# Optimization experiments

Measured on AMD Instinct MI355X. Metric: run time of the kernel, lower is better.

## Reference

```python
import jax, jax.numpy as jnp
import numpy as np

B, D_IN, D_H, H = 8192, 1024, 1024, 4
HD = D_H // H          # 256 head dim
D_P = int(D_H * 4 / 3) # 1365 projection dim


def setup_inputs() -> dict:
    key = jax.random.key(0)
    ks = jax.random.split(key, 16)
    s = 0.02
    inp = {
        'x': jax.random.normal(ks[0], (B, D_IN), jnp.float32),
        'h_prev': jnp.zeros((B, D_H), jnp.float32),
        'c_prev': jnp.zeros((B, D_H), jnp.float32),
        'n_prev': jnp.zeros((B, D_H), jnp.float32),
        'm_prev': jnp.zeros((B, D_H), jnp.float32),
        'ln_w': jnp.ones((D_IN,), jnp.float32),
        'ln_b': jnp.zeros((D_IN,), jnp.float32),
        'Wz': jax.random.normal(ks[1], (D_IN, D_H)) * s,
        'bz': jnp.zeros((D_H,)),
        'Wi': jax.random.normal(ks[2], (D_IN, D_H)) * s,
        'bi': jnp.zeros((D_H,)),
        'Wf': jax.random.normal(ks[3], (D_IN, D_H)) * s,
        'bf': jnp.zeros((D_H,)),
        'Wo': jax.random.normal(ks[4], (D_IN, D_H)) * s,
        'bo': jnp.zeros((D_H,)),
        'Rz': jax.random.normal(ks[5], (H, HD, HD)) * s,
        'rbz': jnp.zeros((D_H,)),
        'Ri': jax.random.normal(ks[6], (H, HD, HD)) * s,
        'rbi': jnp.zeros((D_H,)),
        'Rf': jax.random.normal(ks[7], (H, HD, HD)) * s,
        'rbf': jnp.zeros((D_H,)),
        'Ro': jax.random.normal(ks[8], (H, HD, HD)) * s,
        'rbo': jnp.zeros((D_H,)),
        'gn_w': jnp.ones((D_H,)),
        'gn_b': jnp.zeros((D_H,)),
        'Wup': jax.random.normal(ks[9], (D_H, 2 * D_P)) * s,
        'bup': jnp.zeros((2 * D_P,)),
        'Wdown': jax.random.normal(ks[10], (D_P, D_IN)) * s,
        'bdown': jnp.zeros((D_IN,)),
    }
    return inp


def reference(x, h_prev, c_prev, n_prev, m_prev,
              ln_w, ln_b,
              Wz, bz, Wi, bi, Wf, bf, Wo, bo,
              Rz, rbz, Ri, rbi, Rf, rbf, Ro, rbo,
              gn_w, gn_b, Wup, bup, Wdown, bdown):
    EPS = 1e-5
    # LayerNorm over input_dim
    mu = x.mean(-1, keepdims=True)
    var = x.var(-1, keepdims=True)
    x_oz = (x - mu) / jnp.sqrt(var + EPS) * ln_w + ln_b
    x_fi = x_oz  # use_conv=False

    # block-diagonal recurrence: per-head (HD x HD) matmul
    hr = h_prev.reshape(B, H, HD)
    def blk(R, rb):
        return jnp.einsum('bhd,hde->bhe', hr, R).reshape(B, D_H) + rb

    z_t = x_oz @ Wz + bz + blk(Rz, rbz)
    i_t = x_fi @ Wi + bi + blk(Ri, rbi)
    f_t = x_fi @ Wf + bf + blk(Rf, rbf)
    o_t = x_fi @ Wo + bo + blk(Ro, rbo)

    zt = jnp.tanh(z_t)
    ot = jax.nn.sigmoid(o_t)
    mt = jnp.maximum(f_t + m_prev, i_t)          # stabilizer
    it = jnp.exp(i_t - mt)
    ft = jnp.exp(f_t + m_prev - mt)
    ct = ft * c_prev + it * zt
    nt = ft * n_prev + it
    ht = ot * (ct / (nt + 1e-13))

    # GroupNorm(num_heads, hidden_dim) on (B, D_H)
    g = ht.reshape(B, H, HD)
    gm = g.mean(-1, keepdims=True)
    gv = g.var(-1, keepdims=True)
    ht_norm = ((g - gm) / jnp.sqrt(gv + EPS)).reshape(B, D_H) * gn_w + gn_b

    # GeGLU feedforward + residual
    up = ht_norm @ Wup + bup
    s_, g_ = up[:, :D_P], up[:, D_P:]
    y = (s_ * jax.nn.gelu(g_, approximate=False)) @ Wdown + bdown + x
    return (y, ht, ct, nt, mt)
```

## Files before the change

### kernel.cpp

```cpp
#include <hip/hip_runtime.h>
#include <hip/hip_bf16.h>
#include <math.h>

#define B_ROWS 8192
#define DIN    1024
#define DH     1024
#define HD     256
#define DP     1365
#define DP2    2730
#define NUP    2816
#define KDN    1408

typedef __bf16 bf16x8 __attribute__((ext_vector_type(8)));
typedef float  f32x4  __attribute__((ext_vector_type(4)));
typedef unsigned short ushort_t;

__device__ __forceinline__ unsigned short f2bf(float f) {
    union { __hip_bfloat16 b; unsigned short u; } v; v.b = __float2bfloat16(f); return v.u;
}
__device__ __forceinline__ float bf2f(unsigned short u) {
    union { __hip_bfloat16 b; unsigned short u; } v; v.u = u; return __bfloat162float(v.b);
}

__global__ __launch_bounds__(256) void prep_hprev(const float* __restrict__ hp,
                                                  ushort_t* __restrict__ out) {
    size_t i = ((size_t)blockIdx.x * 256 + threadIdx.x) * 8;
    float4 a = *(const float4*)(hp + i);
    float4 b = *(const float4*)(hp + i + 4);
    union { unsigned short s[8]; uint4 v; } o;
    o.s[0] = f2bf(a.x); o.s[1] = f2bf(a.y); o.s[2] = f2bf(a.z); o.s[3] = f2bf(a.w);
    o.s[4] = f2bf(b.x); o.s[5] = f2bf(b.y); o.s[6] = f2bf(b.z); o.s[7] = f2bf(b.w);
    *(uint4*)(out + i) = o.v;
}

__global__ __launch_bounds__(256) void prep_wgates(
    const float* __restrict__ Wz, const float* __restrict__ Wi,
    const float* __restrict__ Wf, const float* __restrict__ Wo,
    const float* __restrict__ Rz, const float* __restrict__ Ri,
    const float* __restrict__ Rf, const float* __restrict__ Ro,
    ushort_t* __restrict__ WT) {
    int g = blockIdx.z;
    const float* W = (g == 0) ? Wz : (g == 1) ? Wi : (g == 2) ? Wf : Wo;
    const float* R = (g == 0) ? Rz : (g == 1) ? Ri : (g == 2) ? Rf : Ro;
    int n  = blockIdx.x * 256 + threadIdx.x;
    int k0 = blockIdx.y * 8;
    union { unsigned short s[8]; uint4 v; } o;
    if (k0 < 1024) {
        #pragma unroll
        for (int j = 0; j < 8; ++j) o.s[j] = f2bf(W[(size_t)(k0 + j) * DH + n]);
    } else {
        int h = n >> 8, e = n & 255, d0 = k0 - 1024;
        #pragma unroll
        for (int j = 0; j < 8; ++j) o.s[j] = f2bf(R[h * 65536 + (d0 + j) * 256 + e]);
    }
    *(uint4*)(WT + (size_t)g * 1024 * 1280 + (size_t)n * 1280 + k0) = o.v;
}

__global__ __launch_bounds__(256) void prep_wup(const float* __restrict__ Wup,
                                                ushort_t* __restrict__ WupT) {
    int n  = blockIdx.x * 256 + threadIdx.x;
    int k0 = blockIdx.y * 8;
    union { unsigned short s[8]; uint4 v; } o;
    #pragma unroll
    for (int j = 0; j < 8; ++j)
        o.s[j] = (n < DP2) ? f2bf(Wup[(size_t)(k0 + j) * DP2 + n]) : (unsigned short)0;
    *(uint4*)(WupT + (size_t)n * 1024 + k0) = o.v;
}

__global__ __launch_bounds__(256) void prep_wdown(const float* __restrict__ Wdown,
                                                  ushort_t* __restrict__ WdnT) {
    int n  = blockIdx.x * 256 + threadIdx.x;
    int k0 = blockIdx.y * 8;
    union { unsigned short s[8]; uint4 v; } o;
    #pragma unroll
    for (int j = 0; j < 8; ++j) {
        int k = k0 + j;
        o.s[j] = (k < DP) ? f2bf(Wdown[(size_t)k * DIN + n]) : (unsigned short)0;
    }
    *(uint4*)(WdnT + (size_t)n * KDN + k0) = o.v;
}

__global__ __launch_bounds__(256) void ln_kernel(const float* __restrict__ x,
                                                 const float* __restrict__ w,
                                                 const float* __restrict__ b,
                                                 ushort_t* __restrict__ xn) {
    int row = blockIdx.x;
    int tid = threadIdx.x;
    const float4 v = *(const float4*)(x + (size_t)row * DIN + tid * 4);
    float s  = v.x + v.y + v.z + v.w;
    float sq = v.x*v.x + v.y*v.y + v.z*v.z + v.w*v.w;
    #pragma unroll
    for (int off = 32; off; off >>= 1) {
        s  += __shfl_xor(s, off);
        sq += __shfl_xor(sq, off);
    }
    __shared__ float ss[8];
    int wid = tid >> 6, lane = tid & 63;
    if (lane == 0) { ss[wid] = s; ss[4 + wid] = sq; }
    __syncthreads();
    s  = ss[0] + ss[1] + ss[2] + ss[3];
    sq = ss[4] + ss[5] + ss[6] + ss[7];
    float mu  = s * (1.0f / DIN);
    float var = sq * (1.0f / DIN) - mu * mu;
    float inv = rsqrtf(var + 1e-5f);
    int c = tid * 4;
    float4 wv = *(const float4*)(w + c);
    float4 bv = *(const float4*)(b + c);
    union { unsigned short s4[4]; uint2 v2; } o;
    o.s4[0] = f2bf((v.x - mu) * inv * wv.x + bv.x);
    o.s4[1] = f2bf((v.y - mu) * inv * wv.y + bv.y);
    o.s4[2] = f2bf((v.z - mu) * inv * wv.z + bv.z);
    o.s4[3] = f2bf((v.w - mu) * inv * wv.w + bv.w);
    *(uint2*)(xn + (size_t)row * DIN + c) = o.v2;
}

__global__ __launch_bounds__(256) void gemm_gates_bf(
    const ushort_t* __restrict__ xn, const ushort_t* __restrict__ hp,
    const ushort_t* __restrict__ WT,
    const float* __restrict__ bz, const float* __restrict__ bi,
    const float* __restrict__ bf_, const float* __restrict__ bo,
    const float* __restrict__ rbz, const float* __restrict__ rbi,
    const float* __restrict__ rbf, const float* __restrict__ rbo,
    ushort_t* __restrict__ gates) {
    int g = blockIdx.z;
    const float* bias = (g == 0) ? bz  : (g == 1) ? bi  : (g == 2) ? bf_ : bo;
    const float* rb   = (g == 0) ? rbz : (g == 1) ? rbi : (g == 2) ? rbf : rbo;
    const ushort_t* Wg = WT + (size_t)g * 1024 * 1280;

    __shared__ __align__(16) ushort_t As[128 * 32];
    __shared__ __align__(16) ushort_t Bs[128 * 32];
    int tid = threadIdx.x, lane = tid & 63, wave = tid >> 6;
    int wm = wave >> 1, wn = wave & 1;
    int m0 = blockIdx.y * 128, n0 = blockIdx.x * 128;
    int head = n0 >> 8;
    int trow = tid >> 2;
    int tk   = (tid & 3) * 8;
    int l15 = lane & 15, l4 = lane >> 4;

    f32x4 acc[4][4];
    #pragma unroll
    for (int i = 0; i < 4; ++i)
        #pragma unroll
        for (int j = 0; j < 4; ++j) acc[i][j] = (f32x4){0.f, 0.f, 0.f, 0.f};

    for (int kt = 0; kt < 40; ++kt) {
        int k0 = kt * 32;
        const ushort_t* ap = (k0 < 1024) ? xn + k0
                                         : hp + head * 256 + (k0 - 1024);
        bf16x8 a0 = *(const bf16x8*)(ap + (size_t)(m0 + trow) * 1024 + tk);
        bf16x8 a1 = *(const bf16x8*)(ap + (size_t)(m0 + trow + 64) * 1024 + tk);
        bf16x8 b0 = *(const bf16x8*)(Wg + (size_t)(n0 + trow) * 1280 + k0 + tk);
        bf16x8 b1 = *(const bf16x8*)(Wg + (size_t)(n0 + trow + 64) * 1280 + k0 + tk);
        __syncthreads();
        *(bf16x8*)(As + trow * 32 + tk)        = a0;
        *(bf16x8*)(As + (trow + 64) * 32 + tk) = a1;
        *(bf16x8*)(Bs + trow * 32 + tk)        = b0;
        *(bf16x8*)(Bs + (trow + 64) * 32 + tk) = b1;
        __syncthreads();
        bf16x8 af[4], bv[4];
        #pragma unroll
        for (int i = 0; i < 4; ++i) {
            af[i] = *(const bf16x8*)(As + (wm * 64 + i * 16 + l15) * 32 + l4 * 8);
            bv[i] = *(const bf16x8*)(Bs + (wn * 64 + i * 16 + l15) * 32 + l4 * 8);
        }
        #pragma unroll
        for (int mi = 0; mi < 4; ++mi)
            #pragma unroll
            for (int ni = 0; ni < 4; ++ni)
                acc[mi][ni] = __builtin_amdgcn_mfma_f32_16x16x32_bf16(af[mi], bv[ni], acc[mi][ni], 0, 0, 0);
    }

    ushort_t* og = gates + (size_t)g * B_ROWS * DH;
    #pragma unroll
    for (int ni = 0; ni < 4; ++ni) {
        int col = n0 + wn * 64 + ni * 16 + l15;
        float badd = bias[col] + rb[col];
        #pragma unroll
        for (int mi = 0; mi < 4; ++mi) {
            int rbase = m0 + wm * 64 + mi * 16 + l4 * 4;
            #pragma unroll
            for (int j = 0; j < 4; ++j)
                og[(size_t)(rbase + j) * DH + col] = f2bf(acc[mi][ni][j] + badd);
        }
    }
}

__global__ __launch_bounds__(256) void pointwise_gn(
    const ushort_t* __restrict__ gbf,
    const float* __restrict__ c_prev, const float* __restrict__ n_prev,
    const float* __restrict__ m_prev, const float* __restrict__ gn_w,
    const float* __restrict__ gn_b, float* __restrict__ out,
    ushort_t* __restrict__ htn) {
    int row = blockIdx.x;
    int tid = threadIdx.x;
    int head = tid >> 6, lane = tid & 63;
    int col = head * HD + lane * 4;
    size_t idx = (size_t)row * DH + col;
    const size_t N = (size_t)B_ROWS * DH;

    float zv[4], ivv[4], fv[4], ov[4];
    {
        union { uint2 v; unsigned short s[4]; } t;
        t.v = *(const uint2*)(gbf + idx);
        for (int j = 0; j < 4; ++j) zv[j] = bf2f(t.s[j]);
        t.v = *(const uint2*)(gbf + N + idx);
        for (int j = 0; j < 4; ++j) ivv[j] = bf2f(t.s[j]);
        t.v = *(const uint2*)(gbf + 2 * N + idx);
        for (int j = 0; j < 4; ++j) fv[j] = bf2f(t.s[j]);
        t.v = *(const uint2*)(gbf + 3 * N + idx);
        for (int j = 0; j < 4; ++j) ov[j] = bf2f(t.s[j]);
    }
    float4 cp = *(const float4*)(c_prev + idx);
    float4 np = *(const float4*)(n_prev + idx);
    float4 mp = *(const float4*)(m_prev + idx);
    float cpv[4] = {cp.x, cp.y, cp.z, cp.w};
    float npv[4] = {np.x, np.y, np.z, np.w};
    float mpv[4] = {mp.x, mp.y, mp.z, mp.w};

    float htv[4], ctv[4], ntv[4], mtv[4];
    float s = 0.f, sq = 0.f;
    #pragma unroll
    for (int j = 0; j < 4; ++j) {
        float zt = tanhf(zv[j]);
        float ot = 1.0f / (1.0f + expf(-ov[j]));
        float mt = fmaxf(fv[j] + mpv[j], ivv[j]);
        float it = expf(ivv[j] - mt);
        float ft = expf(fv[j] + mpv[j] - mt);
        float ct = ft * cpv[j] + it * zt;
        float nt = ft * npv[j] + it;
        float h  = ot * (ct / (nt + 1e-13f));
        htv[j] = h; ctv[j] = ct; ntv[j] = nt; mtv[j] = mt;
        s += h; sq += h * h;
    }
    *(float4*)(out + N     + idx) = make_float4(htv[0], htv[1], htv[2], htv[3]);
    *(float4*)(out + 2 * N + idx) = make_float4(ctv[0], ctv[1], ctv[2], ctv[3]);
    *(float4*)(out + 3 * N + idx) = make_float4(ntv[0], ntv[1], ntv[2], ntv[3]);
    *(float4*)(out + 4 * N + idx) = make_float4(mtv[0], mtv[1], mtv[2], mtv[3]);

    #pragma unroll
    for (int off = 1; off < 64; off <<= 1) {
        s  += __shfl_xor(s, off);
        sq += __shfl_xor(sq, off);
    }
    float mean = s * (1.0f / HD);
    float var  = fmaxf(sq * (1.0f / HD) - mean * mean, 0.0f);
    float inv  = rsqrtf(var + 1e-5f);
    float4 gw = *(const float4*)(gn_w + col);
    float4 gb = *(const float4*)(gn_b + col);
    float gwv[4] = {gw.x, gw.y, gw.z, gw.w};
    float gbv[4] = {gb.x, gb.y, gb.z, gb.w};
    union { unsigned short s4[4]; uint2 v2; } o;
    #pragma unroll
    for (int j = 0; j < 4; ++j)
        o.s4[j] = f2bf((htv[j] - mean) * inv * gwv[j] + gbv[j]);
    *(uint2*)(htn + idx) = o.v2;
}

__global__ __launch_bounds__(256) void gemm_up_bf(const ushort_t* __restrict__ htn,
                                                  const ushort_t* __restrict__ WupT,
                                                  const float* __restrict__ bup,
                                                  ushort_t* __restrict__ up) {
    __shared__ __align__(16) ushort_t As[128 * 32];
    __shared__ __align__(16) ushort_t Bs[128 * 32];
    int tid = threadIdx.x, lane = tid & 63, wave = tid >> 6;
    int wm = wave >> 1, wn = wave & 1;
    int m0 = blockIdx.y * 128, n0 = blockIdx.x * 128;
    int trow = tid >> 2;
    int tk   = (tid & 3) * 8;
    int l15 = lane & 15, l4 = lane >> 4;

    f32x4 acc[4][4];
    #pragma unroll
    for (int i = 0; i < 4; ++i)
        #pragma unroll
        for (int j = 0; j < 4; ++j) acc[i][j] = (f32x4){0.f, 0.f, 0.f, 0.f};

    for (int kt = 0; kt < 32; ++kt) {
        int k0 = kt * 32;
        bf16x8 a0 = *(const bf16x8*)(htn  + (size_t)(m0 + trow) * 1024 + k0 + tk);
        bf16x8 a1 = *(const bf16x8*)(htn  + (size_t)(m0 + trow + 64) * 1024 + k0 + tk);
        bf16x8 b0 = *(const bf16x8*)(WupT + (size_t)(n0 + trow) * 1024 + k0 + tk);
        bf16x8 b1 = *(const bf16x8*)(WupT + (size_t)(n0 + trow + 64) * 1024 + k0 + tk);
        __syncthreads();
        *(bf16x8*)(As + trow * 32 + tk)        = a0;
        *(bf16x8*)(As + (trow + 64) * 32 + tk) = a1;
        *(bf16x8*)(Bs + trow * 32 + tk)        = b0;
        *(bf16x8*)(Bs + (trow + 64) * 32 + tk) = b1;
        __syncthreads();
        bf16x8 af[4], bv[4];
        #pragma unroll
        for (int i = 0; i < 4; ++i) {
            af[i] = *(const bf16x8*)(As + (wm * 64 + i * 16 + l15) * 32 + l4 * 8);
            bv[i] = *(const bf16x8*)(Bs + (wn * 64 + i * 16 + l15) * 32 + l4 * 8);
        }
        #pragma unroll
        for (int mi = 0; mi < 4; ++mi)
            #pragma unroll
            for (int ni = 0; ni < 4; ++ni)
                acc[mi][ni] = __builtin_amdgcn_mfma_f32_16x16x32_bf16(af[mi], bv[ni], acc[mi][ni], 0, 0, 0);
    }

    #pragma unroll
    for (int ni = 0; ni < 4; ++ni) {
        int col = n0 + wn * 64 + ni * 16 + l15;
        float badd = (col < DP2) ? bup[col] : 0.f;
        #pragma unroll
        for (int mi = 0; mi < 4; ++mi) {
            int rbase = m0 + wm * 64 + mi * 16 + l4 * 4;
            #pragma unroll
            for (int j = 0; j < 4; ++j)
                up[(size_t)(rbase + j) * NUP + col] = f2bf(acc[mi][ni][j] + badd);
        }
    }
}

__global__ __launch_bounds__(256) void gelu_kernel(const ushort_t* __restrict__ up,
                                                   ushort_t* __restrict__ act) {
    int row = blockIdx.y;
    int c = blockIdx.x * 256 + threadIdx.x;
    if (c >= KDN) return;
    float v = 0.f;
    if (c < DP) {
        float s = bf2f(up[(size_t)row * NUP + c]);
        float g = bf2f(up[(size_t)row * NUP + DP + c]);
        v = s * 0.5f * g * (1.0f + erff(g * 0.70710678118654752f));
    }
    act[(size_t)row * KDN + c] = f2bf(v);
}

__global__ __launch_bounds__(256) void gemm_down_bf(const ushort_t* __restrict__ act,
                                                    const ushort_t* __restrict__ WdnT,
                                                    const float* __restrict__ bdown,
                                                    const float* __restrict__ x,
                                                    float* __restrict__ y) {
    __shared__ __align__(16) ushort_t As[128 * 32];
    __shared__ __align__(16) ushort_t Bs[128 * 32];
    int tid = threadIdx.x, lane = tid & 63, wave = tid >> 6;
    int wm = wave >> 1, wn = wave & 1;
    int m0 = blockIdx.y * 128, n0 = blockIdx.x * 128;
    int trow = tid >> 2;
    int tk   = (tid & 3) * 8;
    int l15 = lane & 15, l4 = lane >> 4;

    f32x4 acc[4][4];
    #pragma unroll
    for (int i = 0; i < 4; ++i)
        #pragma unroll
        for (int j = 0; j < 4; ++j) acc[i][j] = (f32x4){0.f, 0.f, 0.f, 0.f};

    for (int kt = 0; kt < 44; ++kt) {
        int k0 = kt * 32;
        bf16x8 a0 = *(const bf16x8*)(act  + (size_t)(m0 + trow) * KDN + k0 + tk);
        bf16x8 a1 = *(const bf16x8*)(act  + (size_t)(m0 + trow + 64) * KDN + k0 + tk);
        bf16x8 b0 = *(const bf16x8*)(WdnT + (size_t)(n0 + trow) * KDN + k0 + tk);
        bf16x8 b1 = *(const bf16x8*)(WdnT + (size_t)(n0 + trow + 64) * KDN + k0 + tk);
        __syncthreads();
        *(bf16x8*)(As + trow * 32 + tk)        = a0;
        *(bf16x8*)(As + (trow + 64) * 32 + tk) = a1;
        *(bf16x8*)(Bs + trow * 32 + tk)        = b0;
        *(bf16x8*)(Bs + (trow + 64) * 32 + tk) = b1;
        __syncthreads();
        bf16x8 af[4], bv[4];
        #pragma unroll
        for (int i = 0; i < 4; ++i) {
            af[i] = *(const bf16x8*)(As + (wm * 64 + i * 16 + l15) * 32 + l4 * 8);
            bv[i] = *(const bf16x8*)(Bs + (wn * 64 + i * 16 + l15) * 32 + l4 * 8);
        }
        #pragma unroll
        for (int mi = 0; mi < 4; ++mi)
            #pragma unroll
            for (int ni = 0; ni < 4; ++ni)
                acc[mi][ni] = __builtin_amdgcn_mfma_f32_16x16x32_bf16(af[mi], bv[ni], acc[mi][ni], 0, 0, 0);
    }

    #pragma unroll
    for (int ni = 0; ni < 4; ++ni) {
        int col = n0 + wn * 64 + ni * 16 + l15;
        float bd = bdown[col];
        #pragma unroll
        for (int mi = 0; mi < 4; ++mi) {
            int rbase = m0 + wm * 64 + mi * 16 + l4 * 4;
            #pragma unroll
            for (int j = 0; j < 4; ++j) {
                int r = rbase + j;
                y[(size_t)r * DIN + col] = acc[mi][ni][j] + bd + x[(size_t)r * DIN + col];
            }
        }
    }
}

extern "C" void kernel_launch(void* const* d_in, const int* in_sizes, int n_in,
                              void* d_out, int out_size, void* d_ws, size_t ws_size,
                              hipStream_t stream) {
    (void)in_sizes; (void)n_in; (void)out_size; (void)ws_size;
    const float* x      = (const float*)d_in[0];
    const float* h_prev = (const float*)d_in[1];
    const float* c_prev = (const float*)d_in[2];
    const float* n_prev = (const float*)d_in[3];
    const float* m_prev = (const float*)d_in[4];
    const float* ln_w   = (const float*)d_in[5];
    const float* ln_b   = (const float*)d_in[6];
    const float* Wz = (const float*)d_in[7];  const float* bz = (const float*)d_in[8];
    const float* Wi = (const float*)d_in[9];  const float* bi = (const float*)d_in[10];
    const float* Wf = (const float*)d_in[11]; const float* bf_ = (const float*)d_in[12];
    const float* Wo = (const float*)d_in[13]; const float* bo = (const float*)d_in[14];
    const float* Rz = (const float*)d_in[15]; const float* rbz = (const float*)d_in[16];
    const float* Ri = (const float*)d_in[17]; const float* rbi = (const float*)d_in[18];
    const float* Rf = (const float*)d_in[19]; const float* rbf = (const float*)d_in[20];
    const float* Ro = (const float*)d_in[21]; const float* rbo = (const float*)d_in[22];
    const float* gn_w = (const float*)d_in[23]; const float* gn_b = (const float*)d_in[24];
    const float* Wup  = (const float*)d_in[25]; const float* bup  = (const float*)d_in[26];
    const float* Wdown = (const float*)d_in[27]; const float* bdown = (const float*)d_in[28];

    char* w = (char*)d_ws;
    ushort_t* hp_bf  = (ushort_t*)(w);
    ushort_t* WTg    = (ushort_t*)(w + 16777216);
    ushort_t* WupT   = (ushort_t*)(w + 27262976);
    ushort_t* WdnT   = (ushort_t*)(w + 33030144);
    ushort_t* xn_bf  = (ushort_t*)(w + 35913728);
    ushort_t* htn_bf = xn_bf;
    char*     big    = w + 52690944;
    ushort_t* gates_bf = (ushort_t*)big;
    ushort_t* up_bf    = (ushort_t*)big;
    ushort_t* act_bf   = (ushort_t*)(big + 46137344);
    float* out = (float*)d_out;

    prep_hprev <<<4096, 256, 0, stream>>>(h_prev, hp_bf);
    prep_wgates<<<dim3(4, 160, 4), 256, 0, stream>>>(Wz, Wi, Wf, Wo, Rz, Ri, Rf, Ro, WTg);
    prep_wup   <<<dim3(11, 128), 256, 0, stream>>>(Wup, WupT);
    prep_wdown <<<dim3(4, 176), 256, 0, stream>>>(Wdown, WdnT);
    ln_kernel  <<<B_ROWS, 256, 0, stream>>>(x, ln_w, ln_b, xn_bf);

    gemm_gates_bf<<<dim3(8, 64, 4), 256, 0, stream>>>(
        xn_bf, hp_bf, WTg, bz, bi, bf_, bo, rbz, rbi, rbf, rbo, gates_bf);

    pointwise_gn<<<B_ROWS, 256, 0, stream>>>(
        gates_bf, c_prev, n_prev, m_prev, gn_w, gn_b, out, htn_bf);

    gemm_up_bf<<<dim3(22, 64), 256, 0, stream>>>(htn_bf, WupT, bup, up_bf);

    gelu_kernel<<<dim3(6, B_ROWS), 256, 0, stream>>>(up_bf, act_bf);

    gemm_down_bf<<<dim3(8, 64), 256, 0, stream>>>(act_bf, WdnT, bdown, x, out);
}
```

Measured before the change: 673.8 us.

## Double-buffer LDS in GEMM kernels, swizzle LDS layout, remap workgroups for L2 locality

All three bf16 MFMA GEMMs now use two LDS buffers, so the global loads for the next k-tile are issued before the MFMAs on the current tile, and there is one barrier per tile instead of two. The LDS layout is changed to a k-group-major arrangement so that fragment reads and writes are contiguous 16-byte chunks, which is meant to cut bank conflicts. Block indices are remapped to interleave workgroups across what appear to be XCDs (stride 8), so that neighbouring tiles share L2. The cost is double the LDS footprint and more live registers, which may reduce occupancy.

```diff
diff --git a/kernel.cpp b/kernel.cpp
--- a/kernel.cpp
+++ b/kernel.cpp
@@ -114,6 +114,7 @@
     *(uint2*)(xn + (size_t)row * DIN + c) = o.v2;
 }
 
+
 __global__ __launch_bounds__(256) void gemm_gates_bf(
     const ushort_t* __restrict__ xn, const ushort_t* __restrict__ hp,
     const ushort_t* __restrict__ WT,
@@ -122,20 +123,25 @@
     const float* __restrict__ rbz, const float* __restrict__ rbi,
     const float* __restrict__ rbf, const float* __restrict__ rbo,
     ushort_t* __restrict__ gates) {
-    int g = blockIdx.z;
+    int bid = blockIdx.x + (blockIdx.y << 3) + (blockIdx.z << 9);
+    int wgs = (bid & 7) * 256 + (bid >> 3);
+    int bxi = wgs & 7, rest = wgs >> 3, byi = rest & 63;
+    int g   = rest >> 6;
     const float* bias = (g == 0) ? bz  : (g == 1) ? bi  : (g == 2) ? bf_ : bo;
     const float* rb   = (g == 0) ? rbz : (g == 1) ? rbi : (g == 2) ? rbf : rbo;
     const ushort_t* Wg = WT + (size_t)g * 1024 * 1280;
 
-    __shared__ __align__(16) ushort_t As[128 * 32];
-    __shared__ __align__(16) ushort_t Bs[128 * 32];
+    __shared__ __align__(16) char Ash[2][8192];
+    __shared__ __align__(16) char Bsh[2][8192];
     int tid = threadIdx.x, lane = tid & 63, wave = tid >> 6;
     int wm = wave >> 1, wn = wave & 1;
-    int m0 = blockIdx.y * 128, n0 = blockIdx.x * 128;
+    int m0 = byi * 128, n0 = bxi * 128;
     int head = n0 >> 8;
-    int trow = tid >> 2;
-    int tk   = (tid & 3) * 8;
+    int trow = tid >> 2, kg = tid & 3, tk = kg * 8;
     int l15 = lane & 15, l4 = lane >> 4;
+    int wa  = ((trow >> 4) << 10) + (kg << 8) + ((trow & 15) << 4);
+    int raA = (wm << 12) + (l4 << 8) + (l15 << 4);
+    int raB = (wn << 12) + (l4 << 8) + (l15 << 4);
 
     f32x4 acc[4][4];
     #pragma unroll
@@ -143,31 +149,56 @@
         #pragma unroll
         for (int j = 0; j < 4; ++j) acc[i][j] = (f32x4){0.f, 0.f, 0.f, 0.f};
 
-    for (int kt = 0; kt < 40; ++kt) {
-        int k0 = kt * 32;
-        const ushort_t* ap = (k0 < 1024) ? xn + k0
-                                         : hp + head * 256 + (k0 - 1024);
-        bf16x8 a0 = *(const bf16x8*)(ap + (size_t)(m0 + trow) * 1024 + tk);
-        bf16x8 a1 = *(const bf16x8*)(ap + (size_t)(m0 + trow + 64) * 1024 + tk);
-        bf16x8 b0 = *(const bf16x8*)(Wg + (size_t)(n0 + trow) * 1280 + k0 + tk);
-        bf16x8 b1 = *(const bf16x8*)(Wg + (size_t)(n0 + trow + 64) * 1280 + k0 + tk);
-        __syncthreads();
-        *(bf16x8*)(As + trow * 32 + tk)        = a0;
-        *(bf16x8*)(As + (trow + 64) * 32 + tk) = a1;
-        *(bf16x8*)(Bs + trow * 32 + tk)        = b0;
-        *(bf16x8*)(Bs + (trow + 64) * 32 + tk) = b1;
-        __syncthreads();
+    const ushort_t* aX = xn + (size_t)(m0 + trow) * 1024 + tk;
+    const ushort_t* aH = hp + (size_t)(m0 + trow) * 1024 + head * 256 + tk;
+    const ushort_t* bW = Wg + (size_t)(n0 + trow) * 1280 + tk;
+
+    auto loadAB = [&](int kt, bf16x8& a0, bf16x8& a1, bf16x8& b0, bf16x8& b1) {
+        const ushort_t* p = (kt < 32) ? aX + kt * 32 : aH + (kt - 32) * 32;
+        a0 = *(const bf16x8*)p;
+        a1 = *(const bf16x8*)(p + 64 * 1024);
+        const ushort_t* q = bW + kt * 32;
+        b0 = *(const bf16x8*)q;
+        b1 = *(const bf16x8*)(q + 64 * 1280);
+    };
+    auto stage = [&](char* A, char* Bb, bf16x8 a0, bf16x8 a1, bf16x8 b0, bf16x8 b1) {
+        *(bf16x8*)(A + wa)         = a0;
+        *(bf16x8*)(A + wa + 4096)  = a1;
+        *(bf16x8*)(Bb + wa)        = b0;
+        *(bf16x8*)(Bb + wa + 4096) = b1;
+    };
+    auto compute = [&](const char* A, const char* Bb) {
         bf16x8 af[4], bv[4];
         #pragma unroll
         for (int i = 0; i < 4; ++i) {
-            af[i] = *(const bf16x8*)(As + (wm * 64 + i * 16 + l15) * 32 + l4 * 8);
-            bv[i] = *(const bf16x8*)(Bs + (wn * 64 + i * 16 + l15) * 32 + l4 * 8);
+            af[i] = *(const bf16x8*)(A  + raA + i * 1024);
+            bv[i] = *(const bf16x8*)(Bb + raB + i * 1024);
         }
         #pragma unroll
         for (int mi = 0; mi < 4; ++mi)
             #pragma unroll
             for (int ni = 0; ni < 4; ++ni)
                 acc[mi][ni] = __builtin_amdgcn_mfma_f32_16x16x32_bf16(af[mi], bv[ni], acc[mi][ni], 0, 0, 0);
+    };
+
+    {
+        bf16x8 a0, a1, b0, b1;
+        loadAB(0, a0, a1, b0, b1);
+        stage(Ash[0], Bsh[0], a0, a1, b0, b1);
+    }
+    __syncthreads();
+    for (int kt = 0; kt < 40; kt += 2) {
+        bf16x8 a0, a1, b0, b1;
+        loadAB(kt + 1, a0, a1, b0, b1);
+        compute(Ash[0], Bsh[0]);
+        stage(Ash[1], Bsh[1], a0, a1, b0, b1);
+        __syncthreads();
+        if (kt + 2 < 40) loadAB(kt + 2, a0, a1, b0, b1);
+        compute(Ash[1], Bsh[1]);
+        if (kt + 2 < 40) {
+            stage(Ash[0], Bsh[0], a0, a1, b0, b1);
+            __syncthreads();
+        }
     }
 
     ushort_t* og = gates + (size_t)g * B_ROWS * DH;
@@ -260,14 +291,20 @@
                                                   const ushort_t* __restrict__ WupT,
                                                   const float* __restrict__ bup,
                                                   ushort_t* __restrict__ up) {
-    __shared__ __align__(16) ushort_t As[128 * 32];
-    __shared__ __align__(16) ushort_t Bs[128 * 32];
+    int bid = blockIdx.x + blockIdx.y * 22;
+    int wgs = (bid & 7) * 176 + (bid >> 3);
+    int bxi = wgs % 22, byi = wgs / 22;
+
+    __shared__ __align__(16) char Ash[2][8192];
+    __shared__ __align__(16) char Bsh[2][8192];
     int tid = threadIdx.x, lane = tid & 63, wave = tid >> 6;
     int wm = wave >> 1, wn = wave & 1;
-    int m0 = blockIdx.y * 128, n0 = blockIdx.x * 128;
-    int trow = tid >> 2;
-    int tk   = (tid & 3) * 8;
+    int m0 = byi * 128, n0 = bxi * 128;
+    int trow = tid >> 2, kg = tid & 3, tk = kg * 8;
     int l15 = lane & 15, l4 = lane >> 4;
+    int wa  = ((trow >> 4) << 10) + (kg << 8) + ((trow & 15) << 4);
+    int raA = (wm << 12) + (l4 << 8) + (l15 << 4);
+    int raB = (wn << 12) + (l4 << 8) + (l15 << 4);
 
     f32x4 acc[4][4];
     #pragma unroll
@@ -275,29 +312,55 @@
         #pragma unroll
         for (int j = 0; j < 4; ++j) acc[i][j] = (f32x4){0.f, 0.f, 0.f, 0.f};
 
-    for (int kt = 0; kt < 32; ++kt) {
-        int k0 = kt * 32;
-        bf16x8 a0 = *(const bf16x8*)(htn  + (size_t)(m0 + trow) * 1024 + k0 + tk);
-        bf16x8 a1 = *(const bf16x8*)(htn  + (size_t)(m0 + trow + 64) * 1024 + k0 + tk);
-        bf16x8 b0 = *(const bf16x8*)(WupT + (size_t)(n0 + trow) * 1024 + k0 + tk);
-        bf16x8 b1 = *(const bf16x8*)(WupT + (size_t)(n0 + trow + 64) * 1024 + k0 + tk);
-        __syncthreads();
-        *(bf16x8*)(As + trow * 32 + tk)        = a0;
-        *(bf16x8*)(As + (trow + 64) * 32 + tk) = a1;
-        *(bf16x8*)(Bs + trow * 32 + tk)        = b0;
-        *(bf16x8*)(Bs + (trow + 64) * 32 + tk) = b1;
-        __syncthreads();
+    const ushort_t* aP = htn  + (size_t)(m0 + trow) * 1024 + tk;
+    const ushort_t* bP = WupT + (size_t)(n0 + trow) * 1024 + tk;
+
+    auto loadAB = [&](int kt, bf16x8& a0, bf16x8& a1, bf16x8& b0, bf16x8& b1) {
+        const ushort_t* p = aP + kt * 32;
+        a0 = *(const bf16x8*)p;
+        a1 = *(const bf16x8*)(p + 64 * 1024);
+        const ushort_t* q = bP + kt * 32;
+        b0 = *(const bf16x8*)q;
+        b1 = *(const bf16x8*)(q + 64 * 1024);
+    };
+    auto stage = [&](char* A, char* Bb, bf16x8 a0, bf16x8 a1, bf16x8 b0, bf16x8 b1) {
+        *(bf16x8*)(A + wa)         = a0;
+        *(bf16x8*)(A + wa + 4096)  = a1;
+        *(bf16x8*)(Bb + wa)        = b0;
+        *(bf16x8*)(Bb + wa + 4096) = b1;
+    };
+    auto compute = [&](const char* A, const char* Bb) {
         bf16x8 af[4], bv[4];
         #pragma unroll
         for (int i = 0; i < 4; ++i) {
-            af[i] = *(const bf16x8*)(As + (wm * 64 + i * 16 + l15) * 32 + l4 * 8);
-            bv[i] = *(const bf16x8*)(Bs + (wn * 64 + i * 16 + l15) * 32 + l4 * 8);
+            af[i] = *(const bf16x8*)(A  + raA + i * 1024);
+            bv[i] = *(const bf16x8*)(Bb + raB + i * 1024);
         }
         #pragma unroll
         for (int mi = 0; mi < 4; ++mi)
             #pragma unroll
             for (int ni = 0; ni < 4; ++ni)
                 acc[mi][ni] = __builtin_amdgcn_mfma_f32_16x16x32_bf16(af[mi], bv[ni], acc[mi][ni], 0, 0, 0);
+    };
+
+    {
+        bf16x8 a0, a1, b0, b1;
+        loadAB(0, a0, a1, b0, b1);
+        stage(Ash[0], Bsh[0], a0, a1, b0, b1);
+    }
+    __syncthreads();
+    for (int kt = 0; kt < 32; kt += 2) {
+        bf16x8 a0, a1, b0, b1;
+        loadAB(kt + 1, a0, a1, b0, b1);
+        compute(Ash[0], Bsh[0]);
+        stage(Ash[1], Bsh[1], a0, a1, b0, b1);
+        __syncthreads();
+        if (kt + 2 < 32) loadAB(kt + 2, a0, a1, b0, b1);
+        compute(Ash[1], Bsh[1]);
+        if (kt + 2 < 32) {
+            stage(Ash[0], Bsh[0], a0, a1, b0, b1);
+            __syncthreads();
+        }
     }
 
     #pragma unroll
@@ -333,14 +396,20 @@
                                                     const float* __restrict__ bdown,
                                                     const float* __restrict__ x,
                                                     float* __restrict__ y) {
-    __shared__ __align__(16) ushort_t As[128 * 32];
-    __shared__ __align__(16) ushort_t Bs[128 * 32];
+    int bid = blockIdx.x + (blockIdx.y << 3);
+    int wgs = (bid & 7) * 64 + (bid >> 3);
+    int bxi = wgs & 7, byi = wgs >> 3;
+
+    __shared__ __align__(16) char Ash[2][8192];
+    __shared__ __align__(16) char Bsh[2][8192];
     int tid = threadIdx.x, lane = tid & 63, wave = tid >> 6;
     int wm = wave >> 1, wn = wave & 1;
-    int m0 = blockIdx.y * 128, n0 = blockIdx.x * 128;
-    int trow = tid >> 2;
-    int tk   = (tid & 3) * 8;
+    int m0 = byi * 128, n0 = bxi * 128;
+    int trow = tid >> 2, kg = tid & 3, tk = kg * 8;
     int l15 = lane & 15, l4 = lane >> 4;
+    int wa  = ((trow >> 4) << 10) + (kg << 8) + ((trow & 15) << 4);
+    int raA = (wm << 12) + (l4 << 8) + (l15 << 4);
+    int raB = (wn << 12) + (l4 << 8) + (l15 << 4);
 
     f32x4 acc[4][4];
     #pragma unroll
@@ -348,29 +417,55 @@
         #pragma unroll
         for (int j = 0; j < 4; ++j) acc[i][j] = (f32x4){0.f, 0.f, 0.f, 0.f};
 
-    for (int kt = 0; kt < 44; ++kt) {
-        int k0 = kt * 32;
-        bf16x8 a0 = *(const bf16x8*)(act  + (size_t)(m0 + trow) * KDN + k0 + tk);
-        bf16x8 a1 = *(const bf16x8*)(act  + (size_t)(m0 + trow + 64) * KDN + k0 + tk);
-        bf16x8 b0 = *(const bf16x8*)(WdnT + (size_t)(n0 + trow) * KDN + k0 + tk);
-        bf16x8 b1 = *(const bf16x8*)(WdnT + (size_t)(n0 + trow + 64) * KDN + k0 + tk);
-        __syncthreads();
-        *(bf16x8*)(As + trow * 32 + tk)        = a0;
-        *(bf16x8*)(As + (trow + 64) * 32 + tk) = a1;
-        *(bf16x8*)(Bs + trow * 32 + tk)        = b0;
-        *(bf16x8*)(Bs + (trow + 64) * 32 + tk) = b1;
-        __syncthreads();
+    const ushort_t* aP = act  + (size_t)(m0 + trow) * KDN + tk;
+    const ushort_t* bP = WdnT + (size_t)(n0 + trow) * KDN + tk;
+
+    auto loadAB = [&](int kt, bf16x8& a0, bf16x8& a1, bf16x8& b0, bf16x8& b1) {
+        const ushort_t* p = aP + kt * 32;
+        a0 = *(const bf16x8*)p;
+        a1 = *(const bf16x8*)(p + 64 * KDN);
+        const ushort_t* q = bP + kt * 32;
+        b0 = *(const bf16x8*)q;
+        b1 = *(const bf16x8*)(q + 64 * KDN);
+    };
+    auto stage = [&](char* A, char* Bb, bf16x8 a0, bf16x8 a1, bf16x8 b0, bf16x8 b1) {
+        *(bf16x8*)(A + wa)         = a0;
+        *(bf16x8*)(A + wa + 4096)  = a1;
+        *(bf16x8*)(Bb + wa)        = b0;
+        *(bf16x8*)(Bb + wa + 4096) = b1;
+    };
+    auto compute = [&](const char* A, const char* Bb) {
         bf16x8 af[4], bv[4];
         #pragma unroll
         for (int i = 0; i < 4; ++i) {
-            af[i] = *(const bf16x8*)(As + (wm * 64 + i * 16 + l15) * 32 + l4 * 8);
-            bv[i] = *(const bf16x8*)(Bs + (wn * 64 + i * 16 + l15) * 32 + l4 * 8);
+            af[i] = *(const bf16x8*)(A  + raA + i * 1024);
+            bv[i] = *(const bf16x8*)(Bb + raB + i * 1024);
         }
         #pragma unroll
         for (int mi = 0; mi < 4; ++mi)
             #pragma unroll
             for (int ni = 0; ni < 4; ++ni)
                 acc[mi][ni] = __builtin_amdgcn_mfma_f32_16x16x32_bf16(af[mi], bv[ni], acc[mi][ni], 0, 0, 0);
+    };
+
+    {
+        bf16x8 a0, a1, b0, b1;
+        loadAB(0, a0, a1, b0, b1);
+        stage(Ash[0], Bsh[0], a0, a1, b0, b1);
+    }
+    __syncthreads();
+    for (int kt = 0; kt < 44; kt += 2) {
+        bf16x8 a0, a1, b0, b1;
+        loadAB(kt + 1, a0, a1, b0, b1);
+        compute(Ash[0], Bsh[0]);
+        stage(Ash[1], Bsh[1], a0, a1, b0, b1);
+        __syncthreads();
+        if (kt + 2 < 44) loadAB(kt + 2, a0, a1, b0, b1);
+        compute(Ash[1], Bsh[1]);
+        if (kt + 2 < 44) {
+            stage(Ash[0], Bsh[0], a0, a1, b0, b1);
+            __syncthreads();
+        }
     }
 
     #pragma unroll
```

New measurement: 645.3 us. 4.2% less time.

## Use shared 256x256 double-buffered MFMA GEMM core with XCD-aware block remap

Applied to the files above, without the earlier changes.

Replaces the three 128x128 single-buffered GEMM kernels with a shared templated 256x256 tile core using 512 threads, 8 waves each computing 128x64. Shared memory is double-buffered so the next K-slice's global loads overlap the current MFMA compute, which drops one barrier per iteration. The LDS layout is swizzled into 16-row chunks, and a block-index remap groups neighbouring tiles onto the same XCD for L2 reuse. The larger tiles raise register pressure and cut grid size (e.g. 512 blocks for gates, 128 for down), which risks lower occupancy and tail effects.

```diff
diff --git a/kernel.cpp b/kernel.cpp
--- a/kernel.cpp
+++ b/kernel.cpp
@@ -114,7 +114,73 @@
     *(uint2*)(xn + (size_t)row * DIN + c) = o.v2;
 }
 
-__global__ __launch_bounds__(256) void gemm_gates_bf(
+template<int NK, int SW>
+__device__ __forceinline__ void gemm_core256(
+    const ushort_t* __restrict__ aP0, const ushort_t* __restrict__ aP1, int lda,
+    const ushort_t* __restrict__ bP, int ldb,
+    char* AshB, char* BshB, f32x4 (&acc)[8][4])
+{
+    int tid = threadIdx.x, lane = tid & 63, wave = tid >> 6;
+    int wm = wave >> 2, wn = wave & 3;
+    int trow = tid >> 1, koff = (tid & 1) * 16;
+    int l15 = lane & 15, l4 = lane >> 4;
+    int wA  = ((trow >> 4) << 10) + ((tid & 1) << 9) + ((trow & 15) << 4);
+    int raA = (wm << 13) + (l4 << 8) + (l15 << 4);
+    int raB = (wn << 12) + (l4 << 8) + (l15 << 4);
+    const ushort_t* aRow0 = aP0 + (size_t)trow * lda + koff;
+    const ushort_t* aRow1 = aP1 + (size_t)trow * lda + koff;
+    const ushort_t* bRow  = bP  + (size_t)trow * ldb + koff;
+
+    auto loadAB = [&](int kt, bf16x8& a0, bf16x8& a1, bf16x8& b0, bf16x8& b1) {
+        const ushort_t* p = (SW >= NK || kt < SW) ? aRow0 + kt * 32
+                                                  : aRow1 + (kt - SW) * 32;
+        a0 = *(const bf16x8*)p;
+        a1 = *(const bf16x8*)(p + 8);
+        const ushort_t* q = bRow + kt * 32;
+        b0 = *(const bf16x8*)q;
+        b1 = *(const bf16x8*)(q + 8);
+    };
+    auto stage = [&](char* A, char* B_, bf16x8 a0, bf16x8 a1, bf16x8 b0, bf16x8 b1) {
+        *(bf16x8*)(A + wA)        = a0;
+        *(bf16x8*)(A + wA + 256)  = a1;
+        *(bf16x8*)(B_ + wA)       = b0;
+        *(bf16x8*)(B_ + wA + 256) = b1;
+    };
+    auto compute = [&](const char* A, const char* B_) {
+        bf16x8 af[8], bv[4];
+        #pragma unroll
+        for (int i = 0; i < 8; ++i) af[i] = *(const bf16x8*)(A + raA + i * 1024);
+        #pragma unroll
+        for (int i = 0; i < 4; ++i) bv[i] = *(const bf16x8*)(B_ + raB + i * 1024);
+        #pragma unroll
+        for (int mi = 0; mi < 8; ++mi)
+            #pragma unroll
+            for (int ni = 0; ni < 4; ++ni)
+                acc[mi][ni] = __builtin_amdgcn_mfma_f32_16x16x32_bf16(af[mi], bv[ni], acc[mi][ni], 0, 0, 0);
+    };
+
+    {
+        bf16x8 a0, a1, b0, b1;
+        loadAB(0, a0, a1, b0, b1);
+        stage(AshB, BshB, a0, a1, b0, b1);
+    }
+    __syncthreads();
+    for (int kt = 0; kt < NK; kt += 2) {
+        bf16x8 a0, a1, b0, b1;
+        loadAB(kt + 1, a0, a1, b0, b1);
+        compute(AshB, BshB);
+        stage(AshB + 16384, BshB + 16384, a0, a1, b0, b1);
+        __syncthreads();
+        if (kt + 2 < NK) loadAB(kt + 2, a0, a1, b0, b1);
+        compute(AshB + 16384, BshB + 16384);
+        if (kt + 2 < NK) {
+            stage(AshB, BshB, a0, a1, b0, b1);
+            __syncthreads();
+        }
+    }
+}
+
+__global__ __launch_bounds__(512, 2) void gemm_gates_bf(
     const ushort_t* __restrict__ xn, const ushort_t* __restrict__ hp,
     const ushort_t* __restrict__ WT,
     const float* __restrict__ bz, const float* __restrict__ bi,
@@ -122,62 +188,38 @@
     const float* __restrict__ rbz, const float* __restrict__ rbi,
     const float* __restrict__ rbf, const float* __restrict__ rbo,
     ushort_t* __restrict__ gates) {
-    int g = blockIdx.z;
+    int bid = blockIdx.x + (blockIdx.y << 2) + (blockIdx.z << 7);
+    int wgs = (bid & 7) * 64 + (bid >> 3);
+    int bxi = wgs & 3, rest = wgs >> 2, byi = rest & 31, g = rest >> 5;
     const float* bias = (g == 0) ? bz  : (g == 1) ? bi  : (g == 2) ? bf_ : bo;
     const float* rb   = (g == 0) ? rbz : (g == 1) ? rbi : (g == 2) ? rbf : rbo;
     const ushort_t* Wg = WT + (size_t)g * 1024 * 1280;
-
-    __shared__ __align__(16) ushort_t As[128 * 32];
-    __shared__ __align__(16) ushort_t Bs[128 * 32];
-    int tid = threadIdx.x, lane = tid & 63, wave = tid >> 6;
-    int wm = wave >> 1, wn = wave & 1;
-    int m0 = blockIdx.y * 128, n0 = blockIdx.x * 128;
-    int head = n0 >> 8;
-    int trow = tid >> 2;
-    int tk   = (tid & 3) * 8;
+    int m0 = byi * 256, n0 = bxi * 256, head = bxi;
+
+    __shared__ __align__(16) char Ash[2][16384];
+    __shared__ __align__(16) char Bsh[2][16384];
+    f32x4 acc[8][4];
+    #pragma unroll
+    for (int i = 0; i < 8; ++i)
+        #pragma unroll
+        for (int j = 0; j < 4; ++j) acc[i][j] = (f32x4){0.f, 0.f, 0.f, 0.f};
+
+    gemm_core256<40, 32>(xn + (size_t)m0 * 1024,
+                         hp + (size_t)m0 * 1024 + head * 256, 1024,
+                         Wg + (size_t)n0 * 1280, 1280,
+                         &Ash[0][0], &Bsh[0][0], acc);
+
+    int lane = threadIdx.x & 63, wave = threadIdx.x >> 6;
+    int wm = wave >> 2, wn = wave & 3;
     int l15 = lane & 15, l4 = lane >> 4;
-
-    f32x4 acc[4][4];
-    #pragma unroll
-    for (int i = 0; i < 4; ++i)
-        #pragma unroll
-        for (int j = 0; j < 4; ++j) acc[i][j] = (f32x4){0.f, 0.f, 0.f, 0.f};
-
-    for (int kt = 0; kt < 40; ++kt) {
-        int k0 = kt * 32;
-        const ushort_t* ap = (k0 < 1024) ? xn + k0
-                                         : hp + head * 256 + (k0 - 1024);
-        bf16x8 a0 = *(const bf16x8*)(ap + (size_t)(m0 + trow) * 1024 + tk);
-        bf16x8 a1 = *(const bf16x8*)(ap + (size_t)(m0 + trow + 64) * 1024 + tk);
-        bf16x8 b0 = *(const bf16x8*)(Wg + (size_t)(n0 + trow) * 1280 + k0 + tk);
-        bf16x8 b1 = *(const bf16x8*)(Wg + (size_t)(n0 + trow + 64) * 1280 + k0 + tk);
-        __syncthreads();
-        *(bf16x8*)(As + trow * 32 + tk)        = a0;
-        *(bf16x8*)(As + (trow + 64) * 32 + tk) = a1;
-        *(bf16x8*)(Bs + trow * 32 + tk)        = b0;
-        *(bf16x8*)(Bs + (trow + 64) * 32 + tk) = b1;
-        __syncthreads();
-        bf16x8 af[4], bv[4];
-        #pragma unroll
-        for (int i = 0; i < 4; ++i) {
-            af[i] = *(const bf16x8*)(As + (wm * 64 + i * 16 + l15) * 32 + l4 * 8);
-            bv[i] = *(const bf16x8*)(Bs + (wn * 64 + i * 16 + l15) * 32 + l4 * 8);
-        }
-        #pragma unroll
-        for (int mi = 0; mi < 4; ++mi)
-            #pragma unroll
-            for (int ni = 0; ni < 4; ++ni)
-                acc[mi][ni] = __builtin_amdgcn_mfma_f32_16x16x32_bf16(af[mi], bv[ni], acc[mi][ni], 0, 0, 0);
-    }
-
     ushort_t* og = gates + (size_t)g * B_ROWS * DH;
     #pragma unroll
     for (int ni = 0; ni < 4; ++ni) {
         int col = n0 + wn * 64 + ni * 16 + l15;
         float badd = bias[col] + rb[col];
         #pragma unroll
-        for (int mi = 0; mi < 4; ++mi) {
-            int rbase = m0 + wm * 64 + mi * 16 + l4 * 4;
+        for (int mi = 0; mi < 8; ++mi) {
+            int rbase = m0 + wm * 128 + mi * 16 + l4 * 4;
             #pragma unroll
             for (int j = 0; j < 4; ++j)
                 og[(size_t)(rbase + j) * DH + col] = f2bf(acc[mi][ni][j] + badd);
@@ -256,57 +298,37 @@
     *(uint2*)(htn + idx) = o.v2;
 }
 
-__global__ __launch_bounds__(256) void gemm_up_bf(const ushort_t* __restrict__ htn,
-                                                  const ushort_t* __restrict__ WupT,
-                                                  const float* __restrict__ bup,
-                                                  ushort_t* __restrict__ up) {
-    __shared__ __align__(16) ushort_t As[128 * 32];
-    __shared__ __align__(16) ushort_t Bs[128 * 32];
-    int tid = threadIdx.x, lane = tid & 63, wave = tid >> 6;
-    int wm = wave >> 1, wn = wave & 1;
-    int m0 = blockIdx.y * 128, n0 = blockIdx.x * 128;
-    int trow = tid >> 2;
-    int tk   = (tid & 3) * 8;
+__global__ __launch_bounds__(512, 2) void gemm_up_bf(const ushort_t* __restrict__ htn,
+                                                     const ushort_t* __restrict__ WupT,
+                                                     const float* __restrict__ bup,
+                                                     ushort_t* __restrict__ up) {
+    int bid = blockIdx.x + blockIdx.y * 11;
+    int wgs = (bid & 7) * 44 + (bid >> 3);
+    int bxi = wgs % 11, byi = wgs / 11;
+    int m0 = byi * 256, n0 = bxi * 256;
+
+    __shared__ __align__(16) char Ash[2][16384];
+    __shared__ __align__(16) char Bsh[2][16384];
+    f32x4 acc[8][4];
+    #pragma unroll
+    for (int i = 0; i < 8; ++i)
+        #pragma unroll
+        for (int j = 0; j < 4; ++j) acc[i][j] = (f32x4){0.f, 0.f, 0.f, 0.f};
+
+    const ushort_t* aP = htn + (size_t)m0 * 1024;
+    gemm_core256<32, 32>(aP, aP, 1024, WupT + (size_t)n0 * 1024, 1024,
+                         &Ash[0][0], &Bsh[0][0], acc);
+
+    int lane = threadIdx.x & 63, wave = threadIdx.x >> 6;
+    int wm = wave >> 2, wn = wave & 3;
     int l15 = lane & 15, l4 = lane >> 4;
-
-    f32x4 acc[4][4];
-    #pragma unroll
-    for (int i = 0; i < 4; ++i)
-        #pragma unroll
-        for (int j = 0; j < 4; ++j) acc[i][j] = (f32x4){0.f, 0.f, 0.f, 0.f};
-
-    for (int kt = 0; kt < 32; ++kt) {
-        int k0 = kt * 32;
-        bf16x8 a0 = *(const bf16x8*)(htn  + (size_t)(m0 + trow) * 1024 + k0 + tk);
-        bf16x8 a1 = *(const bf16x8*)(htn  + (size_t)(m0 + trow + 64) * 1024 + k0 + tk);
-        bf16x8 b0 = *(const bf16x8*)(WupT + (size_t)(n0 + trow) * 1024 + k0 + tk);
-        bf16x8 b1 = *(const bf16x8*)(WupT + (size_t)(n0 + trow + 64) * 1024 + k0 + tk);
-        __syncthreads();
-        *(bf16x8*)(As + trow * 32 + tk)        = a0;
-        *(bf16x8*)(As + (trow + 64) * 32 + tk) = a1;
-        *(bf16x8*)(Bs + trow * 32 + tk)        = b0;
-        *(bf16x8*)(Bs + (trow + 64) * 32 + tk) = b1;
-        __syncthreads();
-        bf16x8 af[4], bv[4];
-        #pragma unroll
-        for (int i = 0; i < 4; ++i) {
-            af[i] = *(const bf16x8*)(As + (wm * 64 + i * 16 + l15) * 32 + l4 * 8);
-            bv[i] = *(const bf16x8*)(Bs + (wn * 64 + i * 16 + l15) * 32 + l4 * 8);
-        }
-        #pragma unroll
-        for (int mi = 0; mi < 4; ++mi)
-            #pragma unroll
-            for (int ni = 0; ni < 4; ++ni)
-                acc[mi][ni] = __builtin_amdgcn_mfma_f32_16x16x32_bf16(af[mi], bv[ni], acc[mi][ni], 0, 0, 0);
-    }
-
     #pragma unroll
     for (int ni = 0; ni < 4; ++ni) {
         int col = n0 + wn * 64 + ni * 16 + l15;
         float badd = (col < DP2) ? bup[col] : 0.f;
         #pragma unroll
-        for (int mi = 0; mi < 4; ++mi) {
-            int rbase = m0 + wm * 64 + mi * 16 + l4 * 4;
+        for (int mi = 0; mi < 8; ++mi) {
+            int rbase = m0 + wm * 128 + mi * 16 + l4 * 4;
             #pragma unroll
             for (int j = 0; j < 4; ++j)
                 up[(size_t)(rbase + j) * NUP + col] = f2bf(acc[mi][ni][j] + badd);
@@ -328,58 +350,38 @@
     act[(size_t)row * KDN + c] = f2bf(v);
 }
 
-__global__ __launch_bounds__(256) void gemm_down_bf(const ushort_t* __restrict__ act,
-                                                    const ushort_t* __restrict__ WdnT,
-                                                    const float* __restrict__ bdown,
-                                                    const float* __restrict__ x,
-                                                    float* __restrict__ y) {
-    __shared__ __align__(16) ushort_t As[128 * 32];
-    __shared__ __align__(16) ushort_t Bs[128 * 32];
-    int tid = threadIdx.x, lane = tid & 63, wave = tid >> 6;
-    int wm = wave >> 1, wn = wave & 1;
-    int m0 = blockIdx.y * 128, n0 = blockIdx.x * 128;
-    int trow = tid >> 2;
-    int tk   = (tid & 3) * 8;
+__global__ __launch_bounds__(512, 2) void gemm_down_bf(const ushort_t* __restrict__ act,
+                                                       const ushort_t* __restrict__ WdnT,
+                                                       const float* __restrict__ bdown,
+                                                       const float* __restrict__ x,
+                                                       float* __restrict__ y) {
+    int bid = blockIdx.x + (blockIdx.y << 2);
+    int wgs = (bid & 7) * 16 + (bid >> 3);
+    int bxi = wgs & 3, byi = wgs >> 2;
+    int m0 = byi * 256, n0 = bxi * 256;
+
+    __shared__ __align__(16) char Ash[2][16384];
+    __shared__ __align__(16) char Bsh[2][16384];
+    f32x4 acc[8][4];
+    #pragma unroll
+    for (int i = 0; i < 8; ++i)
+        #pragma unroll
+        for (int j = 0; j < 4; ++j) acc[i][j] = (f32x4){0.f, 0.f, 0.f, 0.f};
+
+    const ushort_t* aP = act + (size_t)m0 * KDN;
+    gemm_core256<44, 44>(aP, aP, KDN, WdnT + (size_t)n0 * KDN, KDN,
+                         &Ash[0][0], &Bsh[0][0], acc);
+
+    int lane = threadIdx.x & 63, wave = threadIdx.x >> 6;
+    int wm = wave >> 2, wn = wave & 3;
     int l15 = lane & 15, l4 = lane >> 4;
-
-    f32x4 acc[4][4];
-    #pragma unroll
-    for (int i = 0; i < 4; ++i)
-        #pragma unroll
-        for (int j = 0; j < 4; ++j) acc[i][j] = (f32x4){0.f, 0.f, 0.f, 0.f};
-
-    for (int kt = 0; kt < 44; ++kt) {
-        int k0 = kt * 32;
-        bf16x8 a0 = *(const bf16x8*)(act  + (size_t)(m0 + trow) * KDN + k0 + tk);
-        bf16x8 a1 = *(const bf16x8*)(act  + (size_t)(m0 + trow + 64) * KDN + k0 + tk);
-        bf16x8 b0 = *(const bf16x8*)(WdnT + (size_t)(n0 + trow) * KDN + k0 + tk);
-        bf16x8 b1 = *(const bf16x8*)(WdnT + (size_t)(n0 + trow + 64) * KDN + k0 + tk);
-        __syncthreads();
-        *(bf16x8*)(As + trow * 32 + tk)        = a0;
-        *(bf16x8*)(As + (trow + 64) * 32 + tk) = a1;
-        *(bf16x8*)(Bs + trow * 32 + tk)        = b0;
-        *(bf16x8*)(Bs + (trow + 64) * 32 + tk) = b1;
-        __syncthreads();
-        bf16x8 af[4], bv[4];
-        #pragma unroll
-        for (int i = 0; i < 4; ++i) {
-            af[i] = *(const bf16x8*)(As + (wm * 64 + i * 16 + l15) * 32 + l4 * 8);
-            bv[i] = *(const bf16x8*)(Bs + (wn * 64 + i * 16 + l15) * 32 + l4 * 8);
-        }
-        #pragma unroll
-        for (int mi = 0; mi < 4; ++mi)
-            #pragma unroll
-            for (int ni = 0; ni < 4; ++ni)
-                acc[mi][ni] = __builtin_amdgcn_mfma_f32_16x16x32_bf16(af[mi], bv[ni], acc[mi][ni], 0, 0, 0);
-    }
-
     #pragma unroll
     for (int ni = 0; ni < 4; ++ni) {
         int col = n0 + wn * 64 + ni * 16 + l15;
         float bd = bdown[col];
         #pragma unroll
-        for (int mi = 0; mi < 4; ++mi) {
-            int rbase = m0 + wm * 64 + mi * 16 + l4 * 4;
+        for (int mi = 0; mi < 8; ++mi) {
+            int rbase = m0 + wm * 128 + mi * 16 + l4 * 4;
             #pragma unroll
             for (int j = 0; j < 4; ++j) {
                 int r = rbase + j;
@@ -431,15 +433,15 @@
     prep_wdown <<<dim3(4, 176), 256, 0, stream>>>(Wdown, WdnT);
     ln_kernel  <<<B_ROWS, 256, 0, stream>>>(x, ln_w, ln_b, xn_bf);
 
-    gemm_gates_bf<<<dim3(8, 64, 4), 256, 0, stream>>>(
+    gemm_gates_bf<<<dim3(4, 32, 4), 512, 0, stream>>>(
         xn_bf, hp_bf, WTg, bz, bi, bf_, bo, rbz, rbi, rbf, rbo, gates_bf);
 
     pointwise_gn<<<B_ROWS, 256, 0, stream>>>(
         gates_bf, c_prev, n_prev, m_prev, gn_w, gn_b, out, htn_bf);
 
-    gemm_up_bf<<<dim3(22, 64), 256, 0, stream>>>(htn_bf, WupT, bup, up_bf);
+    gemm_up_bf<<<dim3(11, 32), 512, 0, stream>>>(htn_bf, WupT, bup, up_bf);
 
     gelu_kernel<<<dim3(6, B_ROWS), 256, 0, stream>>>(up_bf, act_bf);
 
-    gemm_down_bf<<<dim3(8, 64), 256, 0, stream>>>(act_bf, WdnT, bdown, x, out);
-}
+    gemm_down_bf<<<dim3(4, 32), 512, 0, stream>>>(act_bf, WdnT, bdown, x, out);
+}
```

Result: no change. 678.8 us (+0.7%).
